# Performance work log

Hardware: AMD Instinct MI355X
Metric: run time of the kernel (lower is better)

## Reference

```python
import jax, jax.numpy as jnp
import numpy as np

WINDOW = 1024  # sliding-window mask_mod: attend to keys within WINDOW behind the query


def setup_inputs() -> dict:
    key = jax.random.key(0)
    B, L, H, E = 2, 2048, 16, 64
    qkv = jax.random.normal(key, (B, L, 3, H, E), dtype=jnp.float32)
    return {"qkv": qkv}


def reference(qkv) -> jnp.ndarray:
    # Training path of FlexAttention.forward (key_cache/val_cache/cache_seqlens = None).
    B, L, _, H, E = qkv.shape
    q = qkv[:, :, 0]  # [b, l, h, e]
    k = qkv[:, :, 1]
    v = qkv[:, :, 2]

    scale = 1.0 / (E ** 0.5)  # flex_attention default softmax scaling
    scores = jnp.einsum("bqhe,bkhe->bhqk", q, k) * scale  # [b, h, q, kv]

    q_idx = jnp.arange(L)[:, None]
    kv_idx = jnp.arange(L)[None, :]
    dist = q_idx - kv_idx  # [q, kv]

    # score_mod: ALiBi bias, slope_h = 2^(-8*(h+1)/H)
    slopes = jnp.exp2(-8.0 * (jnp.arange(H, dtype=jnp.float32) + 1.0) / H)
    scores = scores - slopes[None, :, None, None] * dist.astype(jnp.float32)

    # and_masks(mask_mod, causal_mask): sliding window AND causal
    mask = (dist >= 0) & (dist < WINDOW)  # causal guarantees >=1 valid key per row
    scores = jnp.where(mask[None, None], scores, -jnp.inf)

    attn = jax.nn.softmax(scores, axis=-1)
    out = jnp.einsum("bhqk,bkhe->bqhe", attn, v)  # [b, l, h, e]
    return out
```

## Files before the change

kernel.cpp:

```cpp
#include <hip/hip_runtime.h>
#include <cstdint>

#define L_SEQ 2048
#define NH 16
#define EDIM 64
#define WINDOW 1024
#define QT 64
#define KT 64
#define LOG2E 1.4426950408889634f
#define M_FIX 16.0f

typedef short bf16x8 __attribute__((ext_vector_type(8)));
typedef short bf16x4 __attribute__((ext_vector_type(4)));
typedef float f32x4 __attribute__((ext_vector_type(4)));

__device__ __forceinline__ short f2bf(float x) {
    uint32_t u = __builtin_bit_cast(uint32_t, x);
    uint32_t r = (u + 0x7fffu + ((u >> 16) & 1u)) >> 16;
    return (short)(r & 0xffffu);
}
__device__ __forceinline__ short f2bf_trunc(float x) {
    return (short)(__builtin_bit_cast(uint32_t, x) >> 16);
}

__device__ __forceinline__ f32x4 mfma16(bf16x4 a, bf16x4 b, f32x4 c) {
#if __has_builtin(__builtin_amdgcn_mfma_f32_16x16x16bf16_1k)
    return __builtin_amdgcn_mfma_f32_16x16x16bf16_1k(a, b, c, 0, 0, 0);
#else
    asm("s_nop 1\n\tv_mfma_f32_16x16x16_bf16 %0, %1, %2, %0"
        : "+v"(c) : "v"(a), "v"(b));
    return c;
#endif
}

__device__ __forceinline__ void async16(const short* g, const short* l) {
    __builtin_amdgcn_global_load_lds(
        (const __attribute__((address_space(1))) void*)(uintptr_t)(g),
        (__attribute__((address_space(3))) void*)(uintptr_t)(l),
        16, 0, 0);
}

__global__ __launch_bounds__(256) void prepass3(const float* __restrict__ qkv,
        short* __restrict__ kw, short* __restrict__ vw) {
    __shared__ float vt[64][68];
    const int x = blockIdx.x;
    const int b = x >> 9, tile = (x >> 4) & 31, h = x & 15;
    const int tid = threadIdx.x;
    const int tg = (b * NH + h) * 32 + tile;
    const float* base = qkv + (size_t)b * (L_SEQ * 3072) + (size_t)tile * 64 * 3072 + h * 64;
    short* ko = kw + (size_t)tg * 4096;
    short* vo = vw + (size_t)tg * 4096;

    #pragma unroll
    for (int it = 0; it < 2; ++it) {
        const int c = tid + it * 256;
        const int row = c >> 3, cc = (c & 7) ^ (row & 7);
        const float* src = base + (size_t)row * 3072 + 1024 + cc * 8;
        float4 a = *(const float4*)src, d = *(const float4*)(src + 4);
        short* o = ko + (size_t)c * 8;
        o[0] = f2bf(a.x); o[1] = f2bf(a.y); o[2] = f2bf(a.z); o[3] = f2bf(a.w);
        o[4] = f2bf(d.x); o[5] = f2bf(d.y); o[6] = f2bf(d.z); o[7] = f2bf(d.w);
    }
    {
        const int row = tid >> 2, e0 = (tid & 3) << 4;
        const float* src = base + (size_t)row * 3072 + 2048 + e0;
        #pragma unroll
        for (int q4 = 0; q4 < 4; ++q4) {
            float4 a = *(const float4*)(src + q4 * 4);
            vt[e0 + q4 * 4 + 0][row] = a.x;
            vt[e0 + q4 * 4 + 1][row] = a.y;
            vt[e0 + q4 * 4 + 2][row] = a.z;
            vt[e0 + q4 * 4 + 3][row] = a.w;
        }
    }
    __syncthreads();
    #pragma unroll
    for (int it = 0; it < 2; ++it) {
        const int c = tid + it * 256;
        const int et = c >> 7, a = (c >> 6) & 1, l6 = c & 63;
        const int quad = l6 >> 4, r16 = l6 & 15;
        const int e = et * 16 + r16;
        float4 x0 = *(const float4*)&vt[e][a * 32 + quad * 4];
        float4 x1 = *(const float4*)&vt[e][a * 32 + 16 + quad * 4];
        bf16x8 o8;
        o8[0] = f2bf(x0.x); o8[1] = f2bf(x0.y); o8[2] = f2bf(x0.z); o8[3] = f2bf(x0.w);
        o8[4] = f2bf(x1.x); o8[5] = f2bf(x1.y); o8[6] = f2bf(x1.z); o8[7] = f2bf(x1.w);
        *(bf16x8*)(vo + (size_t)c * 8) = o8;
    }
}

__global__ __launch_bounds__(256, 4) void flexattn_fwd5(
        const float* __restrict__ qkv, const short* __restrict__ kw,
        const short* __restrict__ vw, float* __restrict__ out) {
    __shared__ __align__(16) short kS[2][4096];
    __shared__ __align__(16) short vS[2][4096];

    const int s = blockIdx.y & 31;
    const int k = blockIdx.y >> 5;
    const int t16 = (s + ((k >> 1) << 4)) & 31;
    const int qtile = (k & 1) ? (31 - t16) : t16;
    const int pairid = blockIdx.x * 4 + k;
    const int h = pairid & 15;
    const int b = pairid >> 4;

    const int tid  = threadIdx.x;
    const int w    = tid >> 6;
    const int lane = tid & 63;
    const int quad = lane >> 4;
    const int r16  = lane & 15;
    const int qb   = qtile * QT;
    const int bh32 = (b * NH + h) * 32;
    const int q    = qb + w * 16 + r16;

    const int t0q = (qb >= WINDOW - 1) ? ((qb - (WINDOW - 1)) >> 6) : 0;
    const int t1  = qtile;
    const int swz = quad ^ (r16 & 7);
    const int cb0 = w * 128;

    {
        const short* ktile = kw + (size_t)(bh32 + t0q) * 4096;
        const short* vtile = vw + (size_t)(bh32 + t0q) * 4096;
        async16(ktile + (size_t)(cb0 + lane) * 8,      &kS[0][cb0 * 8]);
        async16(ktile + (size_t)(cb0 + 64 + lane) * 8, &kS[0][(cb0 + 64) * 8]);
        async16(vtile + (size_t)(cb0 + lane) * 8,      &vS[0][cb0 * 8]);
        async16(vtile + (size_t)(cb0 + 64 + lane) * 8, &vS[0][(cb0 + 64) * 8]);
    }

    const float qscale = 0.125f * LOG2E;
    bf16x8 qfrag[2];
    {
        const float* qrow = qkv + (size_t)b * (L_SEQ * 3072) + (size_t)q * 3072 + h * 64;
        #pragma unroll
        for (int es = 0; es < 2; ++es) {
            const float* p = qrow + es * 32 + quad * 8;
            float4 a = *(const float4*)p;
            float4 c = *(const float4*)(p + 4);
            bf16x8 f;
            f[0] = f2bf(a.x * qscale); f[1] = f2bf(a.y * qscale);
            f[2] = f2bf(a.z * qscale); f[3] = f2bf(a.w * qscale);
            f[4] = f2bf(c.x * qscale); f[5] = f2bf(c.y * qscale);
            f[6] = f2bf(c.z * qscale); f[7] = f2bf(c.w * qscale);
            qfrag[es] = f;
        }
    }

    const float slope2 = __builtin_amdgcn_exp2f(-8.0f * (float)(h + 1) / (float)NH) * LOG2E;
    float E[16];
    #pragma unroll
    for (int ct = 0; ct < 4; ++ct)
        #pragma unroll
        for (int r = 0; r < 4; ++r)
            E[ct * 4 + r] = slope2 * (float)(ct * 16 + quad * 4 + r - q) - M_FIX;

    f32x4 O[4] = {{0,0,0,0},{0,0,0,0},{0,0,0,0},{0,0,0,0}};
    float rs = 0.f;

    for (int kt = t0q; kt <= t1; ++kt) {
        const int cur = (kt - t0q) & 1;
        __syncthreads();
        if (kt < t1) {
            const int nb = cur ^ 1;
            const short* ktile = kw + (size_t)(bh32 + kt + 1) * 4096;
            const short* vtile = vw + (size_t)(bh32 + kt + 1) * 4096;
            async16(ktile + (size_t)(cb0 + lane) * 8,      &kS[nb][cb0 * 8]);
            async16(ktile + (size_t)(cb0 + 64 + lane) * 8, &kS[nb][(cb0 + 64) * 8]);
            async16(vtile + (size_t)(cb0 + lane) * 8,      &vS[nb][cb0 * 8]);
            async16(vtile + (size_t)(cb0 + 64 + lane) * 8, &vS[nb][(cb0 + 64) * 8]);
        }

        f32x4 S[4];
        #pragma unroll
        for (int ct = 0; ct < 4; ++ct) {
            const int c0 = ((ct * 16 + r16) << 3) + swz;
            bf16x8 k0 = *(const bf16x8*)&kS[cur][c0 * 8];
            bf16x8 k1 = *(const bf16x8*)&kS[cur][(c0 ^ 4) * 8];
            f32x4 acc = {0.f, 0.f, 0.f, 0.f};
            acc = __builtin_amdgcn_mfma_f32_16x16x32_bf16(k0, qfrag[0], acc, 0, 0, 0);
            acc = __builtin_amdgcn_mfma_f32_16x16x32_bf16(k1, qfrag[1], acc, 0, 0, 0);
            S[ct] = acc;
        }

        const float At = slope2 * (float)(kt * 64);
        bf16x4 pb[4];
        if (kt != t0q && kt != t1) {
            #pragma unroll
            for (int ct = 0; ct < 4; ++ct)
                #pragma unroll
                for (int r = 0; r < 4; ++r) {
                    const float pe = __builtin_amdgcn_exp2f(S[ct][r] + E[ct * 4 + r] + At);
                    rs += pe;
                    pb[ct][r] = f2bf_trunc(pe);
                }
        } else {
            const int key0 = kt * 64 + quad * 4;
            #pragma unroll
            for (int ct = 0; ct < 4; ++ct)
                #pragma unroll
                for (int r = 0; r < 4; ++r) {
                    const int dist = q - (key0 + ct * 16 + r);
                    float pe = __builtin_amdgcn_exp2f(S[ct][r] + E[ct * 4 + r] + At);
                    pe = (dist < 0 || dist >= WINDOW) ? 0.0f : pe;
                    rs += pe;
                    pb[ct][r] = f2bf_trunc(pe);
                }
        }

        #pragma unroll
        for (int et = 0; et < 4; ++et) {
            #pragma unroll
            for (int a = 0; a < 2; ++a) {
                bf16x8 v8 = *(const bf16x8*)&vS[cur][(size_t)((et * 2 + a) * 64 + lane) * 8];
                bf16x4 vlo = {v8[0], v8[1], v8[2], v8[3]};
                bf16x4 vhi = {v8[4], v8[5], v8[6], v8[7]};
                O[et] = mfma16(vlo, pb[a * 2 + 0], O[et]);
                O[et] = mfma16(vhi, pb[a * 2 + 1], O[et]);
            }
        }
    }

    rs += __shfl_xor(rs, 16, 64);
    rs += __shfl_xor(rs, 32, 64);
    const float rl = 1.0f / rs;

    float* op = out + ((size_t)b * L_SEQ + q) * (NH * EDIM) + h * EDIM;
    #pragma unroll
    for (int et = 0; et < 4; ++et) {
        float4 o4 = {O[et][0] * rl, O[et][1] * rl, O[et][2] * rl, O[et][3] * rl};
        *(float4*)(op + et * 16 + quad * 4) = o4;
    }
}

__global__ __launch_bounds__(256, 2) void flexattn_fwd_fb(
        const float* __restrict__ qkv, float* __restrict__ out) {
    __shared__ __align__(16) short kT[KT * 72];
    __shared__ __align__(16) short vB[8 * 64 * 8];
    __shared__ __align__(16) short pT[4][16 * 72];

    const int qtile = blockIdx.x;
    const int h     = blockIdx.y;
    const int b     = blockIdx.z;
    const int tid   = threadIdx.x;
    const int w     = tid >> 6;
    const int lane  = tid & 63;
    const int quad  = lane >> 4;
    const int r16   = lane & 15;
    const int qb = qtile * QT;
    const int rowstride = 3 * NH * EDIM;

    const float* qbase = qkv + ((size_t)b * L_SEQ * 3 + 0) * (NH * EDIM) + h * EDIM;
    const float* kbase = qkv + ((size_t)b * L_SEQ * 3 + 1) * (NH * EDIM) + h * EDIM;
    const float* vbase = qkv + ((size_t)b * L_SEQ * 3 + 2) * (NH * EDIM) + h * EDIM;

    const float qscale = 0.125f * LOG2E;
    bf16x8 qfrag[2];
    {
        const int qg = qb + w * 16 + r16;
        const float* qrow = qbase + (size_t)qg * rowstride;
        #pragma unroll
        for (int es = 0; es < 2; ++es) {
            const float* p = qrow + es * 32 + quad * 8;
            float4 a = *(const float4*)p;
            float4 c = *(const float4*)(p + 4);
            bf16x8 f;
            f[0] = f2bf(a.x * qscale); f[1] = f2bf(a.y * qscale);
            f[2] = f2bf(a.z * qscale); f[3] = f2bf(a.w * qscale);
            f[4] = f2bf(c.x * qscale); f[5] = f2bf(c.y * qscale);
            f[6] = f2bf(c.z * qscale); f[7] = f2bf(c.w * qscale);
            qfrag[es] = f;
        }
    }

    const float slope2 = __builtin_amdgcn_exp2f(-8.0f * (float)(h + 1) / (float)NH) * LOG2E;
    f32x4 O[4] = {{0,0,0,0},{0,0,0,0},{0,0,0,0},{0,0,0,0}};
    float m_run[4] = {-1e30f, -1e30f, -1e30f, -1e30f};
    float l_run[4] = {0.f, 0.f, 0.f, 0.f};

    const int kmin = (qb >= WINDOW - 1) ? (qb - (WINDOW - 1)) : 0;
    const int t0 = kmin >> 6;
    const int t1 = qtile;

    for (int kt = t0; kt <= t1; ++kt) {
        __syncthreads();
        {
            const int j = tid >> 2;
            const int ebase = (tid & 3) * 16;
            const float* krow = kbase + (size_t)(kt * KT + j) * rowstride + ebase;
            const float* vrow = vbase + (size_t)(kt * KT + j) * rowstride + ebase;
            const int js = j >> 5, qd = (j >> 3) & 3, ii = j & 7;
            #pragma unroll
            for (int ee = 0; ee < 4; ++ee) {
                const int e = ebase + ee * 4;
                float4 k4 = *(const float4*)(krow + ee * 4);
                short* kd = &kT[j * 72 + e];
                kd[0] = f2bf(k4.x); kd[1] = f2bf(k4.y);
                kd[2] = f2bf(k4.z); kd[3] = f2bf(k4.w);
                float4 v4 = *(const float4*)(vrow + ee * 4);
                const int et = e >> 4;
                const int ln = qd * 16 + (e & 15);
                short* vd = &vB[(((js * 4 + et) * 64) + ln) * 8 + ii];
                vd[0]  = f2bf(v4.x);
                vd[8]  = f2bf(v4.y);
                vd[16] = f2bf(v4.z);
                vd[24] = f2bf(v4.w);
            }
        }
        __syncthreads();

        f32x4 S[4];
        #pragma unroll
        for (int ct = 0; ct < 4; ++ct) {
            const short* kr = &kT[(ct * 16 + r16) * 72 + quad * 8];
            bf16x8 b0 = *(const bf16x8*)kr;
            bf16x8 b1 = *(const bf16x8*)(kr + 32);
            f32x4 acc = {0.f, 0.f, 0.f, 0.f};
            acc = __builtin_amdgcn_mfma_f32_16x16x32_bf16(qfrag[0], b0, acc, 0, 0, 0);
            acc = __builtin_amdgcn_mfma_f32_16x16x32_bf16(qfrag[1], b1, acc, 0, 0, 0);
            S[ct] = acc;
        }

        const int q0 = qb + w * 16 + quad * 4;
        float p[4][4];
        float mt[4] = {-1e30f, -1e30f, -1e30f, -1e30f};
        #pragma unroll
        for (int ct = 0; ct < 4; ++ct) {
            const int kg = kt * KT + ct * 16 + r16;
            #pragma unroll
            for (int r = 0; r < 4; ++r) {
                const int dist = q0 + r - kg;
                float s2 = S[ct][r] - slope2 * (float)dist;
                if (dist < 0 || dist >= WINDOW) s2 = -1e30f;
                p[ct][r] = s2;
                mt[r] = fmaxf(mt[r], s2);
            }
        }
        #pragma unroll
        for (int d = 1; d < 16; d <<= 1) {
            #pragma unroll
            for (int r = 0; r < 4; ++r)
                mt[r] = fmaxf(mt[r], __shfl_xor(mt[r], d, 64));
        }

        float alpha[4], rsum[4];
        #pragma unroll
        for (int r = 0; r < 4; ++r) {
            const float mn = fmaxf(m_run[r], mt[r]);
            alpha[r] = __builtin_amdgcn_exp2f(m_run[r] - mn);
            m_run[r] = mn;
            float sacc = 0.f;
            #pragma unroll
            for (int ct = 0; ct < 4; ++ct) {
                const float pe = __builtin_amdgcn_exp2f(p[ct][r] - mn);
                p[ct][r] = pe;
                sacc += pe;
            }
            rsum[r] = sacc;
        }
        #pragma unroll
        for (int d = 1; d < 16; d <<= 1) {
            #pragma unroll
            for (int r = 0; r < 4; ++r)
                rsum[r] += __shfl_xor(rsum[r], d, 64);
        }
        #pragma unroll
        for (int r = 0; r < 4; ++r)
            l_run[r] = l_run[r] * alpha[r] + rsum[r];
        #pragma unroll
        for (int et = 0; et < 4; ++et) {
            #pragma unroll
            for (int r = 0; r < 4; ++r)
                O[et][r] *= alpha[r];
        }

        short* pw = &pT[w][0];
        #pragma unroll
        for (int ct = 0; ct < 4; ++ct) {
            #pragma unroll
            for (int r = 0; r < 4; ++r)
                pw[(quad * 4 + r) * 72 + ct * 16 + r16] = f2bf(p[ct][r]);
        }
        bf16x8 aP0 = *(const bf16x8*)(pw + r16 * 72 + quad * 8);
        bf16x8 aP1 = *(const bf16x8*)(pw + r16 * 72 + 32 + quad * 8);

        #pragma unroll
        for (int et = 0; et < 4; ++et) {
            bf16x8 v0 = *(const bf16x8*)(&vB[((0 * 4 + et) * 64 + lane) * 8]);
            O[et] = __builtin_amdgcn_mfma_f32_16x16x32_bf16(aP0, v0, O[et], 0, 0, 0);
            bf16x8 v1 = *(const bf16x8*)(&vB[((1 * 4 + et) * 64 + lane) * 8]);
            O[et] = __builtin_amdgcn_mfma_f32_16x16x32_bf16(aP1, v1, O[et], 0, 0, 0);
        }
    }

    float* obase = out + (((size_t)b * L_SEQ) * NH + (size_t)h) * EDIM;
    #pragma unroll
    for (int r = 0; r < 4; ++r) {
        const int qg = qb + w * 16 + quad * 4 + r;
        const float rl = 1.0f / l_run[r];
        float* orow = obase + (size_t)qg * (NH * EDIM);
        #pragma unroll
        for (int et = 0; et < 4; ++et)
            orow[et * 16 + r16] = O[et][r] * rl;
    }
}

extern "C" void kernel_launch(void* const* d_in, const int* in_sizes, int n_in,
                              void* d_out, int out_size, void* d_ws, size_t ws_size,
                              hipStream_t stream) {
    const float* qkv = (const float*)d_in[0];
    float* out = (float*)d_out;
    const size_t need = (size_t)2 * 1024 * 4096 * sizeof(short);
    if (ws_size >= need) {
        short* kw = (short*)d_ws;
        short* vw = kw + (size_t)1024 * 4096;
        prepass3<<<1024, 256, 0, stream>>>(qkv, kw, vw);
        dim3 grid(8, 128);
        flexattn_fwd5<<<grid, 256, 0, stream>>>(qkv, kw, vw, out);
    } else {
        dim3 gridfb(L_SEQ / QT, NH, 2);
        flexattn_fwd_fb<<<gridfb, 256, 0, stream>>>(qkv, out);
    }
}
```

Measured before the change: 111.5 us.

## Process two query groups per wave with 128-thread blocks and fold bias into MFMA

The attention kernel now runs 2 waves per block, each handling 32 query rows (two 16-row groups). Each K/V fragment read from LDS is reused for both groups, halving LDS reads per MFMA. The ALiBi bias is preloaded as the MFMA accumulator and advanced by a constant per key tile, which removes the per-element adds before exp2. The prepass block index is remapped so that blocks for one (batch, head) pair group together across XCDs. This costs more registers per wave and fewer waves per block, which may lower occupancy and latency hiding.

Result: slower. 116.5 us (+4.5%).

```diff
diff --git a/kernel.cpp b/kernel.cpp
--- a/kernel.cpp
+++ b/kernel.cpp
@@ -40,13 +40,16 @@
         16, 0, 0);
 }
 
-__global__ __launch_bounds__(256) void prepass3(const float* __restrict__ qkv,
+__global__ __launch_bounds__(256) void prepass4(const float* __restrict__ qkv,
         short* __restrict__ kw, short* __restrict__ vw) {
     __shared__ float vt[64][68];
     const int x = blockIdx.x;
-    const int b = x >> 9, tile = (x >> 4) & 31, h = x & 15;
+    const int xcd = x & 7, y = x >> 3;
+    const int pairid = xcd * 4 + (y >> 5);
+    const int tile = y & 31;
+    const int b = pairid >> 4, h = pairid & 15;
     const int tid = threadIdx.x;
-    const int tg = (b * NH + h) * 32 + tile;
+    const int tg = pairid * 32 + tile;
     const float* base = qkv + (size_t)b * (L_SEQ * 3072) + (size_t)tile * 64 * 3072 + h * 64;
     short* ko = kw + (size_t)tg * 4096;
     short* vo = vw + (size_t)tg * 4096;
@@ -89,7 +92,7 @@
     }
 }
 
-__global__ __launch_bounds__(256, 4) void flexattn_fwd5(
+__global__ __launch_bounds__(128, 2) void flexattn_fwd6(
         const float* __restrict__ qkv, const short* __restrict__ kw,
         const short* __restrict__ vw, float* __restrict__ out) {
     __shared__ __align__(16) short kS[2][4096];
@@ -110,26 +113,30 @@
     const int r16  = lane & 15;
     const int qb   = qtile * QT;
     const int bh32 = (b * NH + h) * 32;
-    const int q    = qb + w * 16 + r16;
+    const int q0   = qb + w * 32 + r16;
 
     const int t0q = (qb >= WINDOW - 1) ? ((qb - (WINDOW - 1)) >> 6) : 0;
     const int t1  = qtile;
     const int swz = quad ^ (r16 & 7);
-    const int cb0 = w * 128;
+    const int cb0 = w * 256;
 
     {
         const short* ktile = kw + (size_t)(bh32 + t0q) * 4096;
         const short* vtile = vw + (size_t)(bh32 + t0q) * 4096;
-        async16(ktile + (size_t)(cb0 + lane) * 8,      &kS[0][cb0 * 8]);
-        async16(ktile + (size_t)(cb0 + 64 + lane) * 8, &kS[0][(cb0 + 64) * 8]);
-        async16(vtile + (size_t)(cb0 + lane) * 8,      &vS[0][cb0 * 8]);
-        async16(vtile + (size_t)(cb0 + 64 + lane) * 8, &vS[0][(cb0 + 64) * 8]);
+        #pragma unroll
+        for (int i = 0; i < 4; ++i) {
+            const int cb = cb0 + i * 64;
+            async16(ktile + (size_t)(cb + lane) * 8, &kS[0][cb * 8]);
+            async16(vtile + (size_t)(cb + lane) * 8, &vS[0][cb * 8]);
+        }
     }
 
     const float qscale = 0.125f * LOG2E;
-    bf16x8 qfrag[2];
-    {
-        const float* qrow = qkv + (size_t)b * (L_SEQ * 3072) + (size_t)q * 3072 + h * 64;
+    bf16x8 qfrag[2][2];
+    #pragma unroll
+    for (int g = 0; g < 2; ++g) {
+        const float* qrow = qkv + (size_t)b * (L_SEQ * 3072)
+                                + (size_t)(q0 + g * 16) * 3072 + h * 64;
         #pragma unroll
         for (int es = 0; es < 2; ++es) {
             const float* p = qrow + es * 32 + quad * 8;
@@ -140,20 +147,24 @@
             f[2] = f2bf(a.z * qscale); f[3] = f2bf(a.w * qscale);
             f[4] = f2bf(c.x * qscale); f[5] = f2bf(c.y * qscale);
             f[6] = f2bf(c.z * qscale); f[7] = f2bf(c.w * qscale);
-            qfrag[es] = f;
+            qfrag[g][es] = f;
         }
     }
 
     const float slope2 = __builtin_amdgcn_exp2f(-8.0f * (float)(h + 1) / (float)NH) * LOG2E;
-    float E[16];
-    #pragma unroll
-    for (int ct = 0; ct < 4; ++ct)
-        #pragma unroll
-        for (int r = 0; r < 4; ++r)
-            E[ct * 4 + r] = slope2 * (float)(ct * 16 + quad * 4 + r - q) - M_FIX;
-
-    f32x4 O[4] = {{0,0,0,0},{0,0,0,0},{0,0,0,0},{0,0,0,0}};
-    float rs = 0.f;
+    const float c64 = slope2 * 64.0f;
+    f32x4 EA[2][4];
+    #pragma unroll
+    for (int g = 0; g < 2; ++g)
+        #pragma unroll
+        for (int ct = 0; ct < 4; ++ct)
+            #pragma unroll
+            for (int r = 0; r < 4; ++r)
+                EA[g][ct][r] = slope2 * (float)(t0q * 64 + ct * 16 + quad * 4 + r
+                                                - (q0 + g * 16)) - M_FIX;
+
+    f32x4 O[2][4] = {};
+    float rs[2] = {0.f, 0.f};
 
     for (int kt = t0q; kt <= t1; ++kt) {
         const int cur = (kt - t0q) & 1;
@@ -162,47 +173,55 @@
             const int nb = cur ^ 1;
             const short* ktile = kw + (size_t)(bh32 + kt + 1) * 4096;
             const short* vtile = vw + (size_t)(bh32 + kt + 1) * 4096;
-            async16(ktile + (size_t)(cb0 + lane) * 8,      &kS[nb][cb0 * 8]);
-            async16(ktile + (size_t)(cb0 + 64 + lane) * 8, &kS[nb][(cb0 + 64) * 8]);
-            async16(vtile + (size_t)(cb0 + lane) * 8,      &vS[nb][cb0 * 8]);
-            async16(vtile + (size_t)(cb0 + 64 + lane) * 8, &vS[nb][(cb0 + 64) * 8]);
-        }
-
-        f32x4 S[4];
+            #pragma unroll
+            for (int i = 0; i < 4; ++i) {
+                const int cb = cb0 + i * 64;
+                async16(ktile + (size_t)(cb + lane) * 8, &kS[nb][cb * 8]);
+                async16(vtile + (size_t)(cb + lane) * 8, &vS[nb][cb * 8]);
+            }
+        }
+
+        f32x4 S[2][4];
         #pragma unroll
         for (int ct = 0; ct < 4; ++ct) {
             const int c0 = ((ct * 16 + r16) << 3) + swz;
             bf16x8 k0 = *(const bf16x8*)&kS[cur][c0 * 8];
             bf16x8 k1 = *(const bf16x8*)&kS[cur][(c0 ^ 4) * 8];
-            f32x4 acc = {0.f, 0.f, 0.f, 0.f};
-            acc = __builtin_amdgcn_mfma_f32_16x16x32_bf16(k0, qfrag[0], acc, 0, 0, 0);
-            acc = __builtin_amdgcn_mfma_f32_16x16x32_bf16(k1, qfrag[1], acc, 0, 0, 0);
-            S[ct] = acc;
-        }
-
-        const float At = slope2 * (float)(kt * 64);
-        bf16x4 pb[4];
+            #pragma unroll
+            for (int g = 0; g < 2; ++g) {
+                f32x4 acc = __builtin_amdgcn_mfma_f32_16x16x32_bf16(k0, qfrag[g][0], EA[g][ct], 0, 0, 0);
+                S[g][ct]  = __builtin_amdgcn_mfma_f32_16x16x32_bf16(k1, qfrag[g][1], acc, 0, 0, 0);
+            }
+        }
+
+        bf16x4 pb[2][4];
         if (kt != t0q && kt != t1) {
             #pragma unroll
-            for (int ct = 0; ct < 4; ++ct)
+            for (int g = 0; g < 2; ++g)
                 #pragma unroll
-                for (int r = 0; r < 4; ++r) {
-                    const float pe = __builtin_amdgcn_exp2f(S[ct][r] + E[ct * 4 + r] + At);
-                    rs += pe;
-                    pb[ct][r] = f2bf_trunc(pe);
-                }
+                for (int ct = 0; ct < 4; ++ct)
+                    #pragma unroll
+                    for (int r = 0; r < 4; ++r) {
+                        const float pe = __builtin_amdgcn_exp2f(S[g][ct][r]);
+                        rs[g] += pe;
+                        pb[g][ct][r] = f2bf_trunc(pe);
+                    }
         } else {
             const int key0 = kt * 64 + quad * 4;
             #pragma unroll
-            for (int ct = 0; ct < 4; ++ct)
+            for (int g = 0; g < 2; ++g) {
+                const int qg = q0 + g * 16;
                 #pragma unroll
-                for (int r = 0; r < 4; ++r) {
-                    const int dist = q - (key0 + ct * 16 + r);
-                    float pe = __builtin_amdgcn_exp2f(S[ct][r] + E[ct * 4 + r] + At);
-                    pe = (dist < 0 || dist >= WINDOW) ? 0.0f : pe;
-                    rs += pe;
-                    pb[ct][r] = f2bf_trunc(pe);
-                }
+                for (int ct = 0; ct < 4; ++ct)
+                    #pragma unroll
+                    for (int r = 0; r < 4; ++r) {
+                        const int dist = qg - (key0 + ct * 16 + r);
+                        float pe = __builtin_amdgcn_exp2f(S[g][ct][r]);
+                        pe = (dist < 0 || dist >= WINDOW) ? 0.0f : pe;
+                        rs[g] += pe;
+                        pb[g][ct][r] = f2bf_trunc(pe);
+                    }
+            }
         }
 
         #pragma unroll
@@ -212,21 +231,34 @@
                 bf16x8 v8 = *(const bf16x8*)&vS[cur][(size_t)((et * 2 + a) * 64 + lane) * 8];
                 bf16x4 vlo = {v8[0], v8[1], v8[2], v8[3]};
                 bf16x4 vhi = {v8[4], v8[5], v8[6], v8[7]};
-                O[et] = mfma16(vlo, pb[a * 2 + 0], O[et]);
-                O[et] = mfma16(vhi, pb[a * 2 + 1], O[et]);
-            }
-        }
-    }
-
-    rs += __shfl_xor(rs, 16, 64);
-    rs += __shfl_xor(rs, 32, 64);
-    const float rl = 1.0f / rs;
-
-    float* op = out + ((size_t)b * L_SEQ + q) * (NH * EDIM) + h * EDIM;
-    #pragma unroll
-    for (int et = 0; et < 4; ++et) {
-        float4 o4 = {O[et][0] * rl, O[et][1] * rl, O[et][2] * rl, O[et][3] * rl};
-        *(float4*)(op + et * 16 + quad * 4) = o4;
+                #pragma unroll
+                for (int g = 0; g < 2; ++g) {
+                    O[g][et] = mfma16(vlo, pb[g][a * 2 + 0], O[g][et]);
+                    O[g][et] = mfma16(vhi, pb[g][a * 2 + 1], O[g][et]);
+                }
+            }
+        }
+
+        #pragma unroll
+        for (int ct = 0; ct < 4; ++ct) {
+            EA[0][ct] += c64;
+            EA[1][ct] += c64;
+        }
+    }
+
+    #pragma unroll
+    for (int g = 0; g < 2; ++g) {
+        float r = rs[g];
+        r += __shfl_xor(r, 16, 64);
+        r += __shfl_xor(r, 32, 64);
+        const float rl = 1.0f / r;
+        float* op = out + ((size_t)b * L_SEQ + (q0 + g * 16)) * (NH * EDIM) + h * EDIM;
+        #pragma unroll
+        for (int et = 0; et < 4; ++et) {
+            float4 o4 = {O[g][et][0] * rl, O[g][et][1] * rl,
+                         O[g][et][2] * rl, O[g][et][3] * rl};
+            *(float4*)(op + et * 16 + quad * 4) = o4;
+        }
     }
 }
 
@@ -411,9 +443,9 @@
     if (ws_size >= need) {
         short* kw = (short*)d_ws;
         short* vw = kw + (size_t)1024 * 4096;
-        prepass3<<<1024, 256, 0, stream>>>(qkv, kw, vw);
+        prepass4<<<1024, 256, 0, stream>>>(qkv, kw, vw);
         dim3 grid(8, 128);
-        flexattn_fwd5<<<grid, 256, 0, stream>>>(qkv, kw, vw, out);
+        flexattn_fwd6<<<grid, 128, 0, stream>>>(qkv, kw, vw, out);
     } else {
         dim3 gridfb(L_SEQ / QT, NH, 2);
         flexattn_fwd_fb<<<gridfb, 256, 0, stream>>>(qkv, out);
```
